# Kernel tuning notes

Hardware: AMD Instinct MI355X
Metric: run time of the kernel (lower is better)

The kernel has to match this reference:

```python
import jax, jax.numpy as jnp
import numpy as np

N_NODES = 100000
N_EDGES = 1600000
HIDDEN_DIM = 64
EIGS_DIM = 32


def setup_inputs() -> dict:
    key = jax.random.key(0)
    k1, k2, k3, k4, k5 = jax.random.split(key, 5)
    q = jax.random.normal(k1, (N_NODES, HIDDEN_DIM), dtype=jnp.float32)
    k = jax.random.normal(k2, (N_NODES, HIDDEN_DIM), dtype=jnp.float32)
    v = jax.random.normal(k3, (N_NODES, HIDDEN_DIM), dtype=jnp.float32)
    eigs = jax.random.normal(k4, (N_NODES, EIGS_DIM), dtype=jnp.float32)
    lambda0 = jnp.zeros((1,), dtype=jnp.float32)  # nn.Parameter(torch.zeros(1))
    indices = jax.random.randint(k5, (2, N_EDGES), 0, N_NODES, dtype=jnp.int64)
    return {"q": q, "k": k, "v": v, "eigs": eigs, "lambda0": lambda0,
            "indices": indices}


def reference(q, k, v, eigs, lambda0, indices):
    n = q.shape[0]
    inv_sqrt_dim = 1.0 / jnp.sqrt(jnp.asarray(q.shape[1], dtype=q.dtype))
    i0 = indices[0]  # destination/row node per edge
    i1 = indices[1]  # source/col node per edge

    # per-edge attention logits: gather-dot-product
    x = jnp.sum(q[i0] * k[i1], axis=-1) * inv_sqrt_dim          # [E]
    y = jnp.sum(eigs[i0] * eigs[i1], axis=-1)                   # [E]
    s = x + jnp.exp(lambda0[0]) * y                             # [E]

    # sparse softmax: clamp(exp(s), -5, 5) then segment-normalize by row sum
    e = jnp.clip(jnp.exp(s), -5.0, 5.0)                         # [E]
    denom = jax.ops.segment_sum(e, i0, num_segments=n)          # [N]
    denom = jnp.where(denom == 0.0, 1.0, denom)
    w = e / denom[i0]                                           # [E]

    # spmm: out[r] = sum_{edges with row r} w_e * v[col_e]
    out = jax.ops.segment_sum(w[:, None] * v[i1], i0, num_segments=n)  # [N, D]
    return out
```

## Files before the change

### kernel.cpp

```cpp
#include <hip/hip_runtime.h>
#include <hip/hip_fp16.h>


#define HD 64
#define ED 32
#define CAP 64
#define RPP 256
#define PSHIFT 8
#define D1 16
#define NB1 1024
#define PCAP 5120
#define SPILL_CAP 131072

struct h4 { __half2 a, b; };

__global__ void p1_bin_kernel(const int* __restrict__ idx, int n_edges,
                              int NP, int chunk,
                              int* __restrict__ part, int* __restrict__ gcur,
                              long long* __restrict__ spill,
                              int* __restrict__ spill_cnt,
                              int* __restrict__ flag,
                              const float* __restrict__ kf,
                              const float* __restrict__ vf,
                              const float* __restrict__ ef,
                              __half* __restrict__ k16,
                              __half* __restrict__ v16,
                              __half* __restrict__ e16,
                              long long nk4, long long ne4) {
    extern __shared__ int sm[];
    int* cnt   = sm;
    int* sbase = sm + NP;
    int* bins  = sm + 2 * NP;
    int tid = threadIdx.x;

    for (int i = tid; i < NP; i += 256) cnt[i] = 0;
    __syncthreads();

    int e0 = blockIdx.x * chunk;
    int n  = n_edges - e0; if (n > chunk) n = chunk; if (n < 0) n = 0;

    for (int i = tid; i < n; i += 256) {
        int e = e0 + i;
        int r = idx[e];
        int c = idx[n_edges + e];
        int p = r >> PSHIFT;
        int w = ((r & (RPP - 1)) << 17) | c;
        int pos = atomicAdd(&cnt[p], 1);
        if (pos < D1) {
            bins[p * D1 + pos] = w;
        } else {
            int s = atomicAdd(spill_cnt, 1);
            if (s < SPILL_CAP) spill[s] = ((long long)r << 32) | (unsigned)c;
            else *flag = 1;
        }
    }
    __syncthreads();

    for (int p = tid; p < NP; p += 256) {
        int m = cnt[p]; if (m > D1) m = D1;
        sbase[p] = (m > 0) ? atomicAdd(&gcur[p], m) : 0;
    }
    __syncthreads();

    int wave = tid >> 6;
    int lane = tid & 63;
    int sg = lane >> 4;
    int sl = lane & 15;
    for (int p0 = wave * 4; p0 < NP; p0 += 16) {
        int p = p0 + sg;
        if (p < NP) {
            int m = cnt[p]; if (m > D1) m = D1;
            if (sl < m) {
                int slot = sbase[p] + sl;
                int w = bins[p * D1 + sl];
                if (slot < PCAP) {
                    part[p * PCAP + slot] = w;
                } else {
                    int r = (p << PSHIFT) | (w >> 17);
                    int c = w & 0x1FFFF;
                    int s = atomicAdd(spill_cnt, 1);
                    if (s < SPILL_CAP) spill[s] = ((long long)r << 32) | (unsigned)c;
                    else *flag = 1;
                }
            }
        }
    }

    if (k16 != nullptr) {
        long long gt = (long long)blockIdx.x * 256 + tid;
        long long gs = (long long)gridDim.x * 256;
        for (long long t = gt; t < nk4; t += gs) {
            float4 f = ((const float4*)kf)[t];
            h4 h;
            h.a = __floats2half2_rn(f.x, f.y);
            h.b = __floats2half2_rn(f.z, f.w);
            ((h4*)k16)[t] = h;
        }
        for (long long t = gt; t < nk4; t += gs) {
            float4 f = ((const float4*)vf)[t];
            h4 h;
            h.a = __floats2half2_rn(f.x, f.y);
            h.b = __floats2half2_rn(f.z, f.w);
            ((h4*)v16)[t] = h;
        }
        for (long long t = gt; t < ne4; t += gs) {
            float4 f = ((const float4*)ef)[t];
            h4 h;
            h.a = __floats2half2_rn(f.x, f.y);
            h.b = __floats2half2_rn(f.z, f.w);
            ((h4*)e16)[t] = h;
        }
    }
}

__global__ void p2_bucket_kernel(const int* __restrict__ part,
                                 const int* __restrict__ gcur,
                                 int* __restrict__ count,
                                 int* __restrict__ bucket, int n_nodes) {
    __shared__ int cnt[RPP / 2];
    __shared__ int win[(RPP / 2) * CAP];
    int tid = threadIdx.x;
    if (tid < RPP / 2) cnt[tid] = 0;
    __syncthreads();

    int p    = blockIdx.x >> 1;
    int half = blockIdx.x & 1;
    int n = gcur[p]; if (n > PCAP) n = PCAP;

    for (int i = tid; i < n; i += 256) {
        int w  = part[p * PCAP + i];
        int rl = w >> 17;
        if ((rl >> 7) != half) continue;
        int rh = rl & 127;
        int c  = w & 0x1FFFF;
        int pos = atomicAdd(&cnt[rh], 1);
        if (pos < CAP) win[(rh << 6) + pos] = c;
    }
    __syncthreads();

    int r0 = (p << PSHIFT) + (half << 7);
    int rows = n_nodes - r0;
    if (rows > RPP / 2) rows = RPP / 2;
    if (rows > 0) {
        int nint4 = rows * (CAP / 4);
        int4* dst = (int4*)(bucket + (long long)r0 * CAP);
        const int4* src = (const int4*)win;
        for (int i = tid; i < nint4; i += 256) dst[i] = src[i];
        if (tid < rows) count[r0 + tid] = cnt[tid];
    }
}

__global__ void spill_or_zero_kernel(const long long* __restrict__ spill,
                                     const int* __restrict__ spill_cnt,
                                     const int* __restrict__ flag,
                                     int* __restrict__ count,
                                     int* __restrict__ bucket, int n_nodes) {
    int stride = gridDim.x * blockDim.x;
    int t0 = blockIdx.x * blockDim.x + threadIdx.x;
    if (*flag) {
        for (int t = t0; t < n_nodes; t += stride) count[t] = 0;
        return;
    }
    int ns = *spill_cnt; if (ns > SPILL_CAP) ns = SPILL_CAP;
    for (int t = t0; t < ns; t += stride) {
        long long wc = spill[t];
        int r = (int)(wc >> 32);
        int c = (int)(wc & 0xFFFFFFFFLL);
        int pos = atomicAdd(&count[r], 1);
        if (pos < CAP) bucket[(long long)r * CAP + pos] = c;
    }
}

__global__ void repair_scatter_kernel(const int* __restrict__ flag,
                                      const int* __restrict__ idx,
                                      int* __restrict__ count,
                                      int* __restrict__ bucket, int n_edges) {
    if (*flag == 0) return;
    int t = blockIdx.x * blockDim.x + threadIdx.x;
    if (t < n_edges) {
        int r = idx[t];
        int c = idx[n_edges + t];
        int p = atomicAdd(&count[r], 1);
        if (p < CAP) bucket[(long long)r * CAP + p] = c;
    }
}

__global__ void bucket_scatter_kernel(const int* __restrict__ idx,
                                      int* __restrict__ count,
                                      int* __restrict__ bucket, int n_edges) {
    int t = blockIdx.x * blockDim.x + threadIdx.x;
    if (t < n_edges) {
        int r = idx[t];
        int c = idx[n_edges + t];
        int p = atomicAdd(&count[r], 1);
        if (p < CAP) bucket[(long long)r * CAP + p] = c;
    }
}

__global__ void row16_kernel(const float* __restrict__ q,
                             const __half* __restrict__ k16,
                             const __half* __restrict__ v16,
                             const float* __restrict__ eigs,
                             const __half* __restrict__ e16,
                             const float* __restrict__ lambda0,
                             const int* __restrict__ counts,
                             const int* __restrict__ col,
                             const float* __restrict__ kf,
                             const float* __restrict__ vf,
                             const int* __restrict__ idx, int n_edges,
                             float* __restrict__ out, int n_nodes) {
    long long tid = (long long)blockIdx.x * blockDim.x + threadIdx.x;
    int r = (int)(tid >> 6);
    if (r >= n_nodes) return;
    int lane = threadIdx.x & 63;
    int sub = lane & 15;
    int grp = lane >> 4;

    int deg = counts[r];
    const float expL = __expf(lambda0[0]);

    if (deg > CAP) {
        float qs = q[(long long)r * HD + lane] * 0.125f;
        float gs = (lane < ED) ? eigs[(long long)r * ED + lane] * expL : 0.f;
        float accs = 0.f, den = 0.f;
        for (int base = 0; base < n_edges; base += 64) {
            int e = base + lane;
            int rr = (e < n_edges) ? idx[e] : -1;
            int cc = (e < n_edges) ? idx[n_edges + e] : 0;
            unsigned long long mm = __ballot(rr == r);
            while (mm) {
                int b = __ffsll(mm) - 1;
                mm &= mm - 1;
                int c = __shfl(cc, b, 64);
                float kb = kf[(long long)c * HD + lane];
                float gb = (lane < ED) ? eigs[(long long)c * ED + lane] : 0.f;
                float s = qs * kb + gs * gb;
                #pragma unroll
                for (int off = 32; off > 0; off >>= 1) s += __shfl_xor(s, off, 64);
                float e1 = fminf(__expf(s), 5.0f);
                den += e1;
                accs += e1 * vf[(long long)c * HD + lane];
            }
        }
        float inv = (den == 0.f) ? 1.f : __frcp_rn(den);
        out[(long long)r * HD + lane] = accs * inv;
        return;
    }

    long long start = (long long)r * CAP;

    float4 qa = *(const float4*)(q    + (long long)r * HD + sub * 4);
    float2 ga = *(const float2*)(eigs + (long long)r * ED + sub * 2);
    qa.x *= 0.125f; qa.y *= 0.125f; qa.z *= 0.125f; qa.w *= 0.125f;
    ga.x *= expL;   ga.y *= expL;

    float4 acc = make_float4(0.f, 0.f, 0.f, 0.f);
    float den = 0.f;

    for (int base = 0; base < deg; base += 64) {
        int m = deg - base; if (m > 64) m = 64;
        int cl = (lane < m) ? col[start + base + lane] : 0;
        for (int j = 0; j < m; j += 16) {
            int c1 = __shfl(cl, j + grp,      64);
            int c2 = __shfl(cl, j + 4 + grp,  64);
            int c3 = __shfl(cl, j + 8 + grp,  64);
            int c4 = __shfl(cl, j + 12 + grp, 64);
            h4 kb1 = *(const h4*)(k16 + (long long)c1 * HD + sub * 4);
            __half2 gh1 = *(const __half2*)(e16 + (long long)c1 * ED + sub * 2);
            h4 vv1 = *(const h4*)(v16 + (long long)c1 * HD + sub * 4);
            h4 kb2 = *(const h4*)(k16 + (long long)c2 * HD + sub * 4);
            __half2 gh2 = *(const __half2*)(e16 + (long long)c2 * ED + sub * 2);
            h4 vv2 = *(const h4*)(v16 + (long long)c2 * HD + sub * 4);
            h4 kb3 = *(const h4*)(k16 + (long long)c3 * HD + sub * 4);
            __half2 gh3 = *(const __half2*)(e16 + (long long)c3 * ED + sub * 2);
            h4 vv3 = *(const h4*)(v16 + (long long)c3 * HD + sub * 4);
            h4 kb4 = *(const h4*)(k16 + (long long)c4 * HD + sub * 4);
            __half2 gh4 = *(const __half2*)(e16 + (long long)c4 * ED + sub * 2);
            h4 vv4 = *(const h4*)(v16 + (long long)c4 * HD + sub * 4);

            float s1 = qa.x*__low2float(kb1.a) + qa.y*__high2float(kb1.a)
                     + qa.z*__low2float(kb1.b) + qa.w*__high2float(kb1.b)
                     + ga.x*__low2float(gh1)   + ga.y*__high2float(gh1);
            float s2 = qa.x*__low2float(kb2.a) + qa.y*__high2float(kb2.a)
                     + qa.z*__low2float(kb2.b) + qa.w*__high2float(kb2.b)
                     + ga.x*__low2float(gh2)   + ga.y*__high2float(gh2);
            float s3 = qa.x*__low2float(kb3.a) + qa.y*__high2float(kb3.a)
                     + qa.z*__low2float(kb3.b) + qa.w*__high2float(kb3.b)
                     + ga.x*__low2float(gh3)   + ga.y*__high2float(gh3);
            float s4 = qa.x*__low2float(kb4.a) + qa.y*__high2float(kb4.a)
                     + qa.z*__low2float(kb4.b) + qa.w*__high2float(kb4.b)
                     + ga.x*__low2float(gh4)   + ga.y*__high2float(gh4);
            #pragma unroll
            for (int off = 8; off > 0; off >>= 1) {
                s1 += __shfl_xor(s1, off, 64);
                s2 += __shfl_xor(s2, off, 64);
                s3 += __shfl_xor(s3, off, 64);
                s4 += __shfl_xor(s4, off, 64);
            }
            float e1 = fminf(__expf(s1), 5.0f);
            float e2 = fminf(__expf(s2), 5.0f);
            float e3 = fminf(__expf(s3), 5.0f);
            float e4 = fminf(__expf(s4), 5.0f);

            if (j + grp < m) {
                den += e1;
                acc.x += e1 * __low2float(vv1.a); acc.y += e1 * __high2float(vv1.a);
                acc.z += e1 * __low2float(vv1.b); acc.w += e1 * __high2float(vv1.b);
            }
            if (j + 4 + grp < m) {
                den += e2;
                acc.x += e2 * __low2float(vv2.a); acc.y += e2 * __high2float(vv2.a);
                acc.z += e2 * __low2float(vv2.b); acc.w += e2 * __high2float(vv2.b);
            }
            if (j + 8 + grp < m) {
                den += e3;
                acc.x += e3 * __low2float(vv3.a); acc.y += e3 * __high2float(vv3.a);
                acc.z += e3 * __low2float(vv3.b); acc.w += e3 * __high2float(vv3.b);
            }
            if (j + 12 + grp < m) {
                den += e4;
                acc.x += e4 * __low2float(vv4.a); acc.y += e4 * __high2float(vv4.a);
                acc.z += e4 * __low2float(vv4.b); acc.w += e4 * __high2float(vv4.b);
            }
        }
    }

    #pragma unroll
    for (int off = 16; off < 64; off <<= 1) {
        acc.x += __shfl_xor(acc.x, off, 64);
        acc.y += __shfl_xor(acc.y, off, 64);
        acc.z += __shfl_xor(acc.z, off, 64);
        acc.w += __shfl_xor(acc.w, off, 64);
        den   += __shfl_xor(den,   off, 64);
    }

    if (grp == 0) {
        float inv = (den == 0.0f) ? 1.0f : __frcp_rn(den);
        float4 o = make_float4(acc.x * inv, acc.y * inv, acc.z * inv, acc.w * inv);
        *(float4*)(out + (long long)r * HD + sub * 4) = o;
    }
}

__global__ void row_kernel(const float* __restrict__ q, const float* __restrict__ k,
                           const float* __restrict__ v, const float* __restrict__ eigs,
                           const float* __restrict__ lambda0,
                           const int* __restrict__ counts,
                           const int* __restrict__ col,
                           const int* __restrict__ idx, int n_edges,
                           float* __restrict__ out, int n_nodes) {
    long long tid = (long long)blockIdx.x * blockDim.x + threadIdx.x;
    int r = (int)(tid >> 6);
    if (r >= n_nodes) return;
    int lane = threadIdx.x & 63;
    int sub = lane & 15;
    int grp = lane >> 4;

    int deg = counts[r];
    const float expL = __expf(lambda0[0]);

    if (deg > CAP) {
        float qs = q[(long long)r * HD + lane] * 0.125f;
        float gs = (lane < ED) ? eigs[(long long)r * ED + lane] * expL : 0.f;
        float accs = 0.f, den = 0.f;
        for (int base = 0; base < n_edges; base += 64) {
            int e = base + lane;
            int rr = (e < n_edges) ? idx[e] : -1;
            int cc = (e < n_edges) ? idx[n_edges + e] : 0;
            unsigned long long mm = __ballot(rr == r);
            while (mm) {
                int b = __ffsll(mm) - 1;
                mm &= mm - 1;
                int c = __shfl(cc, b, 64);
                float kb = k[(long long)c * HD + lane];
                float gb = (lane < ED) ? eigs[(long long)c * ED + lane] : 0.f;
                float s = qs * kb + gs * gb;
                #pragma unroll
                for (int off = 32; off > 0; off >>= 1) s += __shfl_xor(s, off, 64);
                float e1 = fminf(__expf(s), 5.0f);
                den += e1;
                accs += e1 * v[(long long)c * HD + lane];
            }
        }
        float inv = (den == 0.f) ? 1.f : __frcp_rn(den);
        out[(long long)r * HD + lane] = accs * inv;
        return;
    }

    long long start = (long long)r * CAP;

    float4 qa = *(const float4*)(q    + (long long)r * HD + sub * 4);
    float2 ga = *(const float2*)(eigs + (long long)r * ED + sub * 2);
    qa.x *= 0.125f; qa.y *= 0.125f; qa.z *= 0.125f; qa.w *= 0.125f;
    ga.x *= expL;   ga.y *= expL;

    float4 acc = make_float4(0.f, 0.f, 0.f, 0.f);
    float den = 0.f;

    for (int base = 0; base < deg; base += 64) {
        int m = deg - base; if (m > 64) m = 64;
        int cl = (lane < m) ? col[start + base + lane] : 0;
        for (int j = 0; j < m; j += 8) {
            int c1 = __shfl(cl, j + grp,     64);
            int c2 = __shfl(cl, j + 4 + grp, 64);
            float4 kb1 = *(const float4*)(k    + (long long)c1 * HD + sub * 4);
            float2 gb1 = *(const float2*)(eigs + (long long)c1 * ED + sub * 2);
            float4 vv1 = *(const float4*)(v    + (long long)c1 * HD + sub * 4);
            float4 kb2 = *(const float4*)(k    + (long long)c2 * HD + sub * 4);
            float2 gb2 = *(const float2*)(eigs + (long long)c2 * ED + sub * 2);
            float4 vv2 = *(const float4*)(v    + (long long)c2 * HD + sub * 4);

            float s1 = qa.x*kb1.x + qa.y*kb1.y + qa.z*kb1.z + qa.w*kb1.w
                     + ga.x*gb1.x + ga.y*gb1.y;
            float s2 = qa.x*kb2.x + qa.y*kb2.y + qa.z*kb2.z + qa.w*kb2.w
                     + ga.x*gb2.x + ga.y*gb2.y;
            #pragma unroll
            for (int off = 8; off > 0; off >>= 1) {
                s1 += __shfl_xor(s1, off, 64);
                s2 += __shfl_xor(s2, off, 64);
            }
            float e1 = fminf(__expf(s1), 5.0f);
            float e2 = fminf(__expf(s2), 5.0f);

            if (j + grp < m) {
                den += e1;
                acc.x += e1 * vv1.x; acc.y += e1 * vv1.y;
                acc.z += e1 * vv1.z; acc.w += e1 * vv1.w;
            }
            if (j + 4 + grp < m) {
                den += e2;
                acc.x += e2 * vv2.x; acc.y += e2 * vv2.y;
                acc.z += e2 * vv2.z; acc.w += e2 * vv2.w;
            }
        }
    }

    #pragma unroll
    for (int off = 16; off < 64; off <<= 1) {
        acc.x += __shfl_xor(acc.x, off, 64);
        acc.y += __shfl_xor(acc.y, off, 64);
        acc.z += __shfl_xor(acc.z, off, 64);
        acc.w += __shfl_xor(acc.w, off, 64);
        den   += __shfl_xor(den,   off, 64);
    }

    if (grp == 0) {
        float inv = (den == 0.0f) ? 1.0f : __frcp_rn(den);
        float4 o = make_float4(acc.x * inv, acc.y * inv, acc.z * inv, acc.w * inv);
        *(float4*)(out + (long long)r * HD + sub * 4) = o;
    }
}

__global__ void edge_fused_kernel(const float* __restrict__ q,
                                  const float* __restrict__ k,
                                  const float* __restrict__ v,
                                  const float* __restrict__ eigs,
                                  const float* __restrict__ lambda0,
                                  const int* __restrict__ idx,
                                  float* __restrict__ denom,
                                  float* __restrict__ out, int n_edges) {
    long long gid = (long long)blockIdx.x * blockDim.x + threadIdx.x;
    int lane = threadIdx.x & 63;
    int edge = (int)(gid >> 4);
    int sub  = (int)(gid & 15);
    int valid = (edge < n_edges);
    int ec = valid ? edge : (n_edges - 1);
    int i0 = idx[ec];
    int i1 = idx[n_edges + ec];
    const float expL = __expf(lambda0[0]);
    float4 qa = *(const float4*)(q + (long long)i0 * HD + sub * 4);
    float4 kb = *(const float4*)(k + (long long)i1 * HD + sub * 4);
    float c = (qa.x*kb.x + qa.y*kb.y + qa.z*kb.z + qa.w*kb.w) * 0.125f;
    float2 ea = *(const float2*)(eigs + (long long)i0 * ED + sub * 2);
    float2 eb = *(const float2*)(eigs + (long long)i1 * ED + sub * 2);
    c += expL * (ea.x * eb.x + ea.y * eb.y);
    #pragma unroll
    for (int off = 8; off > 0; off >>= 1) c += __shfl_xor(c, off, 64);
    float e = fminf(__expf(c), 5.0f);
    if (valid && sub == 0) atomicAdd(&denom[i0], e);
    #pragma unroll
    for (int j = 0; j < 4; ++j) {
        float ej = __shfl(e,     j * 16, 64);
        int   r  = __shfl(i0,    j * 16, 64);
        int   s  = __shfl(i1,    j * 16, 64);
        int   vj = __shfl(valid, j * 16, 64);
        if (vj) {
            float vv = v[(long long)s * HD + lane];
            atomicAdd(&out[(long long)r * HD + lane], ej * vv);
        }
    }
}

__global__ void normalize_kernel(float* __restrict__ out,
                                 const float* __restrict__ denom, int n_nodes) {
    int t = blockIdx.x * blockDim.x + threadIdx.x;
    int total = n_nodes * (HD / 4);
    if (t >= total) return;
    int row = t >> 4;
    float d = denom[row];
    float inv = (d == 0.0f) ? 1.0f : __frcp_rn(d);
    float4* o4 = (float4*)out;
    float4 x = o4[t];
    x.x *= inv; x.y *= inv; x.z *= inv; x.w *= inv;
    o4[t] = x;
}

extern "C" void kernel_launch(void* const* d_in, const int* in_sizes, int n_in,
                              void* d_out, int out_size, void* d_ws, size_t ws_size,
                              hipStream_t stream) {
    const float* q       = (const float*)d_in[0];
    const float* k       = (const float*)d_in[1];
    const float* v       = (const float*)d_in[2];
    const float* eigs    = (const float*)d_in[3];
    const float* lambda0 = (const float*)d_in[4];
    const int*   idx     = (const int*)d_in[5];

    const int n_edges = in_sizes[5] / 2;
    const int n_nodes = in_sizes[0] / HD;

    const int NP = (n_nodes + RPP - 1) / RPP;
    const int eb = (n_edges + 255) / 256;
    long long rthreads = (long long)n_nodes * 64;
    const int rb = (int)((rthreads + 255) / 256);

    size_t ints1 = ((size_t)n_nodes + (size_t)n_nodes * CAP
                    + (size_t)NP * PCAP + NP + 2) * sizeof(int);
    size_t need1  = ints1 + 8 + (size_t)SPILL_CAP * sizeof(long long);
    size_t h16    = (size_t)n_nodes * (HD + HD + ED) * sizeof(__half);
    size_t need16 = h16 + need1;
    size_t need2  = ((size_t)n_nodes + (size_t)n_nodes * CAP) * sizeof(int);

    if (ws_size >= need16) {
        char* base = (char*)d_ws;
        __half* k16 = (__half*)base;
        __half* v16 = k16 + (size_t)n_nodes * HD;
        __half* e16 = v16 + (size_t)n_nodes * HD;
        int* count     = (int*)(e16 + (size_t)n_nodes * ED);
        int* bucket    = count + n_nodes;
        int* part      = bucket + (size_t)n_nodes * CAP;
        int* gcur      = part + (size_t)NP * PCAP;
        int* spill_cnt = gcur + NP;
        int* flag      = spill_cnt + 1;
        size_t soff = (size_t)((char*)(flag + 1) - base);
        soff = (soff + 7) & ~(size_t)7;
        long long* spill = (long long*)(base + soff);

        hipMemsetAsync(gcur, 0, (size_t)(NP + 2) * sizeof(int), stream);

        int chunk = (n_edges + NB1 - 1) / NB1;
        size_t smbytes = (size_t)NP * (2 + D1) * sizeof(int);
        p1_bin_kernel<<<NB1, 256, smbytes, stream>>>(
            idx, n_edges, NP, chunk, part, gcur, spill, spill_cnt, flag,
            k, v, eigs, k16, v16, e16,
            (long long)n_nodes * HD / 4, (long long)n_nodes * ED / 4);
        p2_bucket_kernel<<<2 * NP, 256, 0, stream>>>(part, gcur, count, bucket,
                                                     n_nodes);
        spill_or_zero_kernel<<<(n_nodes + 255) / 256, 256, 0, stream>>>(
            spill, spill_cnt, flag, count, bucket, n_nodes);
        repair_scatter_kernel<<<eb, 256, 0, stream>>>(flag, idx, count, bucket,
                                                      n_edges);
        row16_kernel<<<rb, 256, 0, stream>>>(q, k16, v16, eigs, e16, lambda0,
                                             count, bucket, k, v, idx, n_edges,
                                             (float*)d_out, n_nodes);
    } else if (ws_size >= need1) {
        char* base = (char*)d_ws;
        int* count     = (int*)base;
        int* bucket    = count + n_nodes;
        int* part      = bucket + (size_t)n_nodes * CAP;
        int* gcur      = part + (size_t)NP * PCAP;
        int* spill_cnt = gcur + NP;
        int* flag      = spill_cnt + 1;
        size_t soff = (size_t)((char*)(flag + 1) - base);
        soff = (soff + 7) & ~(size_t)7;
        long long* spill = (long long*)(base + soff);

        hipMemsetAsync(gcur, 0, (size_t)(NP + 2) * sizeof(int), stream);

        int chunk = (n_edges + NB1 - 1) / NB1;
        size_t smbytes = (size_t)NP * (2 + D1) * sizeof(int);
        p1_bin_kernel<<<NB1, 256, smbytes, stream>>>(
            idx, n_edges, NP, chunk, part, gcur, spill, spill_cnt, flag,
            nullptr, nullptr, nullptr, nullptr, nullptr, nullptr, 0, 0);
        p2_bucket_kernel<<<2 * NP, 256, 0, stream>>>(part, gcur, count, bucket,
                                                     n_nodes);
        spill_or_zero_kernel<<<(n_nodes + 255) / 256, 256, 0, stream>>>(
            spill, spill_cnt, flag, count, bucket, n_nodes);
        repair_scatter_kernel<<<eb, 256, 0, stream>>>(flag, idx, count, bucket,
                                                      n_edges);
        row_kernel<<<rb, 256, 0, stream>>>(q, k, v, eigs, lambda0, count, bucket,
                                           idx, n_edges, (float*)d_out, n_nodes);
    } else if (ws_size >= need2) {
        int* count  = (int*)d_ws;
        int* bucket = count + n_nodes;
        hipMemsetAsync(count, 0, (size_t)n_nodes * sizeof(int), stream);
        bucket_scatter_kernel<<<eb, 256, 0, stream>>>(idx, count, bucket, n_edges);
        row_kernel<<<rb, 256, 0, stream>>>(q, k, v, eigs, lambda0, count, bucket,
                                           idx, n_edges, (float*)d_out, n_nodes);
    } else {
        float* denom = (float*)d_ws;
        hipMemsetAsync(denom, 0, (size_t)n_nodes * sizeof(float), stream);
        hipMemsetAsync(d_out, 0, (size_t)out_size * sizeof(float), stream);
        long long threads = (long long)n_edges * 16;
        int grid = (int)((threads + 255) / 256);
        edge_fused_kernel<<<grid, 256, 0, stream>>>(q, k, v, eigs, lambda0, idx,
                                                    denom, (float*)d_out, n_edges);
        int n4 = n_nodes * (HD / 4);
        normalize_kernel<<<(n4 + 255) / 256, 256, 0, stream>>>((float*)d_out,
                                                               denom, n_nodes);
    }
}
```

Before: 263.4 us.

## Replace global atomic partition cursors with fixed per-block slices in binning

The first binning pass no longer reserves space in each partition through global atomicAdd cursors. Each block now writes a fixed 16-int slice per partition: a count header plus up to 15 packed edges. The bucket pass scans every block's slice and reads the count with a shuffle. This removes the global atomics and the gcur memset, but the bucket pass must read NP*nb*16 ints, including empty slots, and the per-block cap drops from 16 to 15 edges, so slightly more edges may spill.

```diff
diff --git a/kernel.cpp b/kernel.cpp
--- a/kernel.cpp
+++ b/kernel.cpp
@@ -7,16 +7,15 @@
 #define CAP 64
 #define RPP 256
 #define PSHIFT 8
-#define D1 16
-#define NB1 1024
-#define PCAP 5120
-#define SPILL_CAP 131072
+#define D1 15
+#define SLICE 16
+#define SPILL_CAP 65536
 
 struct h4 { __half2 a, b; };
 
 __global__ void p1_bin_kernel(const int* __restrict__ idx, int n_edges,
-                              int NP, int chunk,
-                              int* __restrict__ part, int* __restrict__ gcur,
+                              int NP, int chunk, int nb, long long pcap,
+                              int* __restrict__ part,
                               long long* __restrict__ spill,
                               int* __restrict__ spill_cnt,
                               int* __restrict__ flag,
@@ -28,9 +27,8 @@
                               __half* __restrict__ e16,
                               long long nk4, long long ne4) {
     extern __shared__ int sm[];
-    int* cnt   = sm;
-    int* sbase = sm + NP;
-    int* bins  = sm + 2 * NP;
+    int* cnt  = sm;
+    int* bins = sm + NP;
     int tid = threadIdx.x;
 
     for (int i = tid; i < NP; i += 256) cnt[i] = 0;
@@ -56,34 +54,14 @@
     }
     __syncthreads();
 
-    for (int p = tid; p < NP; p += 256) {
+    int g16 = tid >> 4;
+    int sl  = tid & 15;
+    for (int p = g16; p < NP; p += 16) {
         int m = cnt[p]; if (m > D1) m = D1;
-        sbase[p] = (m > 0) ? atomicAdd(&gcur[p], m) : 0;
-    }
-    __syncthreads();
-
-    int wave = tid >> 6;
-    int lane = tid & 63;
-    int sg = lane >> 4;
-    int sl = lane & 15;
-    for (int p0 = wave * 4; p0 < NP; p0 += 16) {
-        int p = p0 + sg;
-        if (p < NP) {
-            int m = cnt[p]; if (m > D1) m = D1;
-            if (sl < m) {
-                int slot = sbase[p] + sl;
-                int w = bins[p * D1 + sl];
-                if (slot < PCAP) {
-                    part[p * PCAP + slot] = w;
-                } else {
-                    int r = (p << PSHIFT) | (w >> 17);
-                    int c = w & 0x1FFFF;
-                    int s = atomicAdd(spill_cnt, 1);
-                    if (s < SPILL_CAP) spill[s] = ((long long)r << 32) | (unsigned)c;
-                    else *flag = 1;
-                }
-            }
-        }
+        long long base = (long long)p * pcap + (long long)blockIdx.x * SLICE;
+        int val = (sl == 0) ? m
+                : (sl <= m) ? bins[p * D1 + sl - 1] : 0;
+        part[base + sl] = val;
     }
 
     if (k16 != nullptr) {
@@ -114,27 +92,34 @@
 }
 
 __global__ void p2_bucket_kernel(const int* __restrict__ part,
-                                 const int* __restrict__ gcur,
                                  int* __restrict__ count,
-                                 int* __restrict__ bucket, int n_nodes) {
-    __shared__ int cnt[RPP / 2];
+                                 int* __restrict__ bucket, int n_nodes,
+                                 int nb, long long pcap) {
+    __shared__ int cnt2[RPP / 2];
     __shared__ int win[(RPP / 2) * CAP];
     int tid = threadIdx.x;
-    if (tid < RPP / 2) cnt[tid] = 0;
+    if (tid < RPP / 2) cnt2[tid] = 0;
     __syncthreads();
 
     int p    = blockIdx.x >> 1;
     int half = blockIdx.x & 1;
-    int n = gcur[p]; if (n > PCAP) n = PCAP;
-
-    for (int i = tid; i < n; i += 256) {
-        int w  = part[p * PCAP + i];
-        int rl = w >> 17;
-        if ((rl >> 7) != half) continue;
-        int rh = rl & 127;
-        int c  = w & 0x1FFFF;
-        int pos = atomicAdd(&cnt[rh], 1);
-        if (pos < CAP) win[(rh << 6) + pos] = c;
+    int g  = tid >> 4;
+    int sl = tid & 15;
+    const int* prow = part + (long long)p * pcap;
+
+    for (int b = g; b < nb; b += 16) {
+        int val = prow[b * SLICE + sl];
+        int m = __shfl(val, 0, 16);
+        if (m > D1) m = D1;
+        if (sl >= 1 && sl <= m) {
+            int rl = val >> 17;
+            if ((rl >> 7) == half) {
+                int rh = rl & 127;
+                int c  = val & 0x1FFFF;
+                int pos = atomicAdd(&cnt2[rh], 1);
+                if (pos < CAP) win[(rh << 6) + pos] = c;
+            }
+        }
     }
     __syncthreads();
 
@@ -146,7 +131,7 @@
         int4* dst = (int4*)(bucket + (long long)r0 * CAP);
         const int4* src = (const int4*)win;
         for (int i = tid; i < nint4; i += 256) dst[i] = src[i];
-        if (tid < rows) count[r0 + tid] = cnt[tid];
+        if (tid < rows) count[r0 + tid] = cnt2[tid];
     }
 }
 
@@ -522,72 +507,73 @@
     long long rthreads = (long long)n_nodes * 64;
     const int rb = (int)((rthreads + 255) / 256);
 
-    size_t ints1 = ((size_t)n_nodes + (size_t)n_nodes * CAP
-                    + (size_t)NP * PCAP + NP + 2) * sizeof(int);
-    size_t need1  = ints1 + 8 + (size_t)SPILL_CAP * sizeof(long long);
-    size_t h16    = (size_t)n_nodes * (HD + HD + ED) * sizeof(__half);
-    size_t need16 = h16 + need1;
-    size_t need2  = ((size_t)n_nodes + (size_t)n_nodes * CAP) * sizeof(int);
-
-    if (ws_size >= need16) {
+    size_t smbytes = (size_t)NP * (1 + D1) * sizeof(int);
+    bool geom_ok = (smbytes <= 60 * 1024) && (n_nodes <= 0x1FFFF);
+
+    size_t fixed = (size_t)n_nodes * sizeof(int)
+                 + (size_t)n_nodes * CAP * sizeof(int);
+    size_t sp = 8 + (size_t)SPILL_CAP * sizeof(long long);
+    size_t h16 = (size_t)n_nodes * (HD + HD + ED) * sizeof(__half);
+
+    auto part_bytes = [&](int nb) {
+        return (size_t)NP * (size_t)nb * SLICE * sizeof(int);
+    };
+    size_t n16_1024 = h16 + fixed + part_bytes(1024) + sp;
+    size_t n16_512  = h16 + fixed + part_bytes(512)  + sp;
+    size_t n32_1024 = fixed + part_bytes(1024) + sp;
+    size_t n32_512  = fixed + part_bytes(512)  + sp;
+    size_t need2    = fixed;
+
+    bool use16 = false;
+    int nb = 0;
+    if (geom_ok && ws_size >= n16_1024)      { use16 = true;  nb = 1024; }
+    else if (geom_ok && ws_size >= n16_512)  { use16 = true;  nb = 512;  }
+    else if (geom_ok && ws_size >= n32_1024) { use16 = false; nb = 1024; }
+    else if (geom_ok && ws_size >= n32_512)  { use16 = false; nb = 512;  }
+
+    if (nb > 0) {
         char* base = (char*)d_ws;
-        __half* k16 = (__half*)base;
-        __half* v16 = k16 + (size_t)n_nodes * HD;
-        __half* e16 = v16 + (size_t)n_nodes * HD;
-        int* count     = (int*)(e16 + (size_t)n_nodes * ED);
-        int* bucket    = count + n_nodes;
-        int* part      = bucket + (size_t)n_nodes * CAP;
-        int* gcur      = part + (size_t)NP * PCAP;
-        int* spill_cnt = gcur + NP;
+        __half* k16 = nullptr; __half* v16 = nullptr; __half* e16 = nullptr;
+        char* ip = base;
+        if (use16) {
+            k16 = (__half*)base;
+            v16 = k16 + (size_t)n_nodes * HD;
+            e16 = v16 + (size_t)n_nodes * HD;
+            ip = (char*)(e16 + (size_t)n_nodes * ED);
+        }
+        int* count  = (int*)ip;
+        int* bucket = count + n_nodes;
+        int* part   = bucket + (size_t)n_nodes * CAP;
+        long long pcap = (long long)nb * SLICE;
+        int* spill_cnt = part + (size_t)NP * pcap;
         int* flag      = spill_cnt + 1;
         size_t soff = (size_t)((char*)(flag + 1) - base);
         soff = (soff + 7) & ~(size_t)7;
         long long* spill = (long long*)(base + soff);
 
-        hipMemsetAsync(gcur, 0, (size_t)(NP + 2) * sizeof(int), stream);
-
-        int chunk = (n_edges + NB1 - 1) / NB1;
-        size_t smbytes = (size_t)NP * (2 + D1) * sizeof(int);
-        p1_bin_kernel<<<NB1, 256, smbytes, stream>>>(
-            idx, n_edges, NP, chunk, part, gcur, spill, spill_cnt, flag,
+        hipMemsetAsync(spill_cnt, 0, 2 * sizeof(int), stream);
+
+        int chunk = (n_edges + nb - 1) / nb;
+        p1_bin_kernel<<<nb, 256, smbytes, stream>>>(
+            idx, n_edges, NP, chunk, nb, pcap, part, spill, spill_cnt, flag,
             k, v, eigs, k16, v16, e16,
-            (long long)n_nodes * HD / 4, (long long)n_nodes * ED / 4);
-        p2_bucket_kernel<<<2 * NP, 256, 0, stream>>>(part, gcur, count, bucket,
-                                                     n_nodes);
+            use16 ? (long long)n_nodes * HD / 4 : 0,
+            use16 ? (long long)n_nodes * ED / 4 : 0);
+        p2_bucket_kernel<<<2 * NP, 256, 0, stream>>>(part, count, bucket,
+                                                     n_nodes, nb, pcap);
         spill_or_zero_kernel<<<(n_nodes + 255) / 256, 256, 0, stream>>>(
             spill, spill_cnt, flag, count, bucket, n_nodes);
         repair_scatter_kernel<<<eb, 256, 0, stream>>>(flag, idx, count, bucket,
                                                       n_edges);
-        row16_kernel<<<rb, 256, 0, stream>>>(q, k16, v16, eigs, e16, lambda0,
-                                             count, bucket, k, v, idx, n_edges,
-                                             (float*)d_out, n_nodes);
-    } else if (ws_size >= need1) {
-        char* base = (char*)d_ws;
-        int* count     = (int*)base;
-        int* bucket    = count + n_nodes;
-        int* part      = bucket + (size_t)n_nodes * CAP;
-        int* gcur      = part + (size_t)NP * PCAP;
-        int* spill_cnt = gcur + NP;
-        int* flag      = spill_cnt + 1;
-        size_t soff = (size_t)((char*)(flag + 1) - base);
-        soff = (soff + 7) & ~(size_t)7;
-        long long* spill = (long long*)(base + soff);
-
-        hipMemsetAsync(gcur, 0, (size_t)(NP + 2) * sizeof(int), stream);
-
-        int chunk = (n_edges + NB1 - 1) / NB1;
-        size_t smbytes = (size_t)NP * (2 + D1) * sizeof(int);
-        p1_bin_kernel<<<NB1, 256, smbytes, stream>>>(
-            idx, n_edges, NP, chunk, part, gcur, spill, spill_cnt, flag,
-            nullptr, nullptr, nullptr, nullptr, nullptr, nullptr, 0, 0);
-        p2_bucket_kernel<<<2 * NP, 256, 0, stream>>>(part, gcur, count, bucket,
-                                                     n_nodes);
-        spill_or_zero_kernel<<<(n_nodes + 255) / 256, 256, 0, stream>>>(
-            spill, spill_cnt, flag, count, bucket, n_nodes);
-        repair_scatter_kernel<<<eb, 256, 0, stream>>>(flag, idx, count, bucket,
-                                                      n_edges);
-        row_kernel<<<rb, 256, 0, stream>>>(q, k, v, eigs, lambda0, count, bucket,
-                                           idx, n_edges, (float*)d_out, n_nodes);
+        if (use16) {
+            row16_kernel<<<rb, 256, 0, stream>>>(q, k16, v16, eigs, e16, lambda0,
+                                                 count, bucket, k, v, idx,
+                                                 n_edges, (float*)d_out, n_nodes);
+        } else {
+            row_kernel<<<rb, 256, 0, stream>>>(q, k, v, eigs, lambda0, count,
+                                               bucket, idx, n_edges,
+                                               (float*)d_out, n_nodes);
+        }
     } else if (ws_size >= need2) {
         int* count  = (int*)d_ws;
         int* bucket = count + n_nodes;
```

Measured after the change: 259.4 us. Within noise of the previous version (-1.5%).
